# Performance work log

Measured on AMD Instinct MI355X. Metric: run time of the kernel, lower is better.

Reference implementation:

```python
import jax, jax.numpy as jnp
import numpy as np
from jax import lax

D_MODEL = 192; PATCH = 16; CH = 3
D_INNER = 384; D_STATE = 16; D_CONV = 4; DT_RANK = 12  # mamba_ssm defaults: expand=2, dt_rank=ceil(d_model/16)


def setup_inputs() -> dict:
    key = jax.random.key(0)
    ks = jax.random.split(key, 12)
    f32 = jnp.float32
    def rn(k, shape, s=0.02):
        return jax.random.normal(k, shape, f32) * s
    return {
        "x": jax.random.uniform(ks[0], (8, 3, 512, 512), f32),
        "patch_w": rn(ks[1], (D_MODEL, CH, PATCH, PATCH)),
        "patch_b": jnp.zeros((D_MODEL,), f32),
        "in_proj_w": rn(ks[2], (2 * D_INNER, D_MODEL)),
        "conv1d_w": rn(ks[3], (D_INNER, 1, D_CONV)),
        "conv1d_b": jnp.zeros((D_INNER,), f32),
        "x_proj_w": rn(ks[4], (DT_RANK + 2 * D_STATE, D_INNER)),
        "dt_proj_w": rn(ks[5], (D_INNER, DT_RANK)),
        "dt_proj_b": rn(ks[6], (D_INNER,), 0.1),
        "A_log": jnp.log(jnp.broadcast_to(jnp.arange(1, D_STATE + 1, dtype=f32), (D_INNER, D_STATE))),
        "D": jnp.ones((D_INNER,), f32),
        "out_proj_w": rn(ks[7], (D_MODEL, D_INNER)),
        "deconv_w": rn(ks[8], (D_MODEL, 64, PATCH, PATCH)),
        "deconv_b": jnp.zeros((64,), f32),
        "dec_conv_w": rn(ks[9], (CH, 64, 3, 3)),
        "dec_conv_b": jnp.zeros((CH,), f32),
    }


def _mamba(seq, in_proj_w, conv1d_w, conv1d_b, x_proj_w, dt_proj_w, dt_proj_b, A_log, D, out_proj_w):
    # seq: (B, L, d_model)
    B, L, _ = seq.shape
    xz = seq @ in_proj_w.T                              # (B, L, 2*d_inner)
    u, z = jnp.split(xz, 2, axis=-1)
    # depthwise causal conv1d (torch pads d_conv-1 both sides then truncates to L == left-pad only)
    uc = lax.conv_general_dilated(u.transpose(0, 2, 1), conv1d_w, (1,), [(D_CONV - 1, 0)],
                                  dimension_numbers=('NCH', 'OIH', 'NCH'),
                                  feature_group_count=D_INNER)       # (B, d_inner, L)
    u = jax.nn.silu((uc + conv1d_b[:, None]).transpose(0, 2, 1))     # (B, L, d_inner)
    dbc = u @ x_proj_w.T                                              # (B, L, dt_rank + 2*d_state)
    dt, Bm, Cm = jnp.split(dbc, [DT_RANK, DT_RANK + D_STATE], axis=-1)
    delta = jax.nn.softplus(dt @ dt_proj_w.T + dt_proj_b)            # (B, L, d_inner)
    A = -jnp.exp(A_log)                                               # (d_inner, d_state)
    dA = jnp.exp(delta[..., None] * A)                                # (B, L, d_inner, d_state)
    dBu = delta[..., None] * Bm[:, :, None, :] * u[..., None]         # (B, L, d_inner, d_state)
    def step(h, inp):
        a, b = inp
        h = a * h + b
        return h, h
    h0 = jnp.zeros((B, D_INNER, D_STATE), seq.dtype)
    _, hs = lax.scan(step, h0, (dA.transpose(1, 0, 2, 3), dBu.transpose(1, 0, 2, 3)))
    y = jnp.einsum('lbdn,bln->bld', hs, Cm) + u * D                   # (B, L, d_inner)
    y = y * jax.nn.silu(z)
    return y @ out_proj_w.T                                           # (B, L, d_model)


def reference(x, patch_w, patch_b, in_proj_w, conv1d_w, conv1d_b, x_proj_w,
              dt_proj_w, dt_proj_b, A_log, D, out_proj_w,
              deconv_w, deconv_b, dec_conv_w, dec_conv_b):
    B = x.shape[0]
    e = lax.conv_general_dilated(x, patch_w, (PATCH, PATCH), 'VALID',
                                 dimension_numbers=('NCHW', 'OIHW', 'NCHW')) + patch_b[:, None, None]
    h, w = e.shape[2], e.shape[3]
    seq = e.reshape(B, D_MODEL, h * w).transpose(0, 2, 1)             # (B, L, d_model)
    seq = _mamba(seq, in_proj_w, conv1d_w, conv1d_b, x_proj_w, dt_proj_w, dt_proj_b, A_log, D, out_proj_w)
    g = seq.transpose(0, 2, 1).reshape(B, D_MODEL, h, w)
    # ConvTranspose2d with stride == kernel_size is a non-overlapping patch expansion
    d = jnp.einsum('bchw,cdpq->bdhpwq', g, deconv_w).reshape(B, 64, h * PATCH, w * PATCH)
    d = jax.nn.relu(d + deconv_b[:, None, None])
    out = lax.conv_general_dilated(d, dec_conv_w, (1, 1), [(1, 1), (1, 1)],
                                   dimension_numbers=('NCHW', 'OIHW', 'NCHW')) + dec_conv_b[:, None, None]
    return jax.nn.sigmoid(out)
```

## Files before the change

kernel.cpp:

```cpp
#include <hip/hip_runtime.h>
#include <math.h>


typedef short bf16x8 __attribute__((ext_vector_type(8)));
typedef float f32x4 __attribute__((ext_vector_type(4)));

__device__ inline unsigned short f2bf(float f) {
    unsigned int u = __float_as_uint(f);
    unsigned int r = (u + 0x7fff + ((u >> 16) & 1)) >> 16;
    return (unsigned short)r;
}

__global__ __launch_bounds__(256) void gemm_mfma_flex(
    const unsigned short* __restrict__ A, const unsigned short* __restrict__ W,
    void* __restrict__ Cout, const float* __restrict__ bias,
    int M, int N, int K, int out_bf16)
{
    __shared__ unsigned short As[128][48];
    __shared__ unsigned short Bs[128][48];
    const int tid = threadIdx.x;
    const int wave = tid >> 6, lane = tid & 63;
    const int wm = (wave & 1) * 64, wn = (wave >> 1) * 64;
    const int m0 = blockIdx.y * 128, n0 = blockIdx.x * 128;
    const int quad = lane >> 4, lr = lane & 15;
    const uint4 z4 = {0, 0, 0, 0};

    f32x4 acc[4][4];
    #pragma unroll
    for (int i = 0; i < 4; ++i)
        #pragma unroll
        for (int j = 0; j < 4; ++j)
            acc[i][j] = (f32x4){0.f, 0.f, 0.f, 0.f};

    const int r = tid >> 2, kq = tid & 3;
    for (int k0 = 0; k0 < K; k0 += 32) {
        #pragma unroll
        for (int half = 0; half < 2; ++half) {
            int rr = r + half * 64;
            *(uint4*)(&As[rr][kq * 8]) =
                *(const uint4*)(A + (size_t)(m0 + rr) * K + k0 + kq * 8);
            uint4 bv = z4;
            if (n0 + rr < N)
                bv = *(const uint4*)(W + (size_t)(n0 + rr) * K + k0 + kq * 8);
            *(uint4*)(&Bs[rr][kq * 8]) = bv;
        }
        __syncthreads();
        bf16x8 af[4], bfr[4];
        #pragma unroll
        for (int i = 0; i < 4; ++i) af[i] = *(const bf16x8*)(&As[wm + i * 16 + lr][quad * 8]);
        #pragma unroll
        for (int j = 0; j < 4; ++j) bfr[j] = *(const bf16x8*)(&Bs[wn + j * 16 + lr][quad * 8]);
        #pragma unroll
        for (int i = 0; i < 4; ++i)
            #pragma unroll
            for (int j = 0; j < 4; ++j)
                acc[i][j] = __builtin_amdgcn_mfma_f32_16x16x32_bf16(af[i], bfr[j], acc[i][j], 0, 0, 0);
        __syncthreads();
    }

    #pragma unroll
    for (int i = 0; i < 4; ++i) {
        int gm = m0 + wm + i * 16 + quad * 4;
        #pragma unroll
        for (int j = 0; j < 4; ++j) {
            int gn = n0 + wn + j * 16 + lr;
            if (gn >= N) continue;
            float bv = bias ? bias[gn] : 0.f;
            #pragma unroll
            for (int rr = 0; rr < 4; ++rr) {
                float v = acc[i][j][rr] + bv;
                if (out_bf16) ((unsigned short*)Cout)[(size_t)(gm + rr) * N + gn] = f2bf(v);
                else          ((float*)Cout)[(size_t)(gm + rr) * N + gn] = v;
            }
        }
    }
}

__global__ __launch_bounds__(256) void gemm_mfma_relu_bf16(
    const unsigned short* __restrict__ A0, const unsigned short* __restrict__ W,
    unsigned short* __restrict__ C0, const float* __restrict__ bias, int pair)
{
    __shared__ unsigned short smem[12288];
    unsigned short* As = smem;
    unsigned short* Bs = smem + 6144;
    const int N = 16384, K = 192;
    const int tid = threadIdx.x;
    const int wave = tid >> 6, lane = tid & 63;
    const int wm = (wave & 1) * 64, wn = (wave >> 1) * 64;
    const int m0 = blockIdx.y * 128, n0 = blockIdx.x * 128;
    const int z = blockIdx.z;
    const unsigned short* A = A0 + (size_t)(pair * 2 + z) * 1024 * 192;
    unsigned short* C = C0 + (size_t)z * 16777216;
    const int quad = lane >> 4, lr = lane & 15;

    f32x4 acc[4][4];
    #pragma unroll
    for (int i = 0; i < 4; ++i)
        #pragma unroll
        for (int j = 0; j < 4; ++j)
            acc[i][j] = (f32x4){0.f, 0.f, 0.f, 0.f};

    const int r = tid >> 2, kq = tid & 3;
    for (int k0 = 0; k0 < K; k0 += 32) {
        #pragma unroll
        for (int half = 0; half < 2; ++half) {
            int rr = r + half * 64;
            *(uint4*)(&As[rr * 48 + kq * 8]) =
                *(const uint4*)(A + (size_t)(m0 + rr) * K + k0 + kq * 8);
            *(uint4*)(&Bs[rr * 48 + kq * 8]) =
                *(const uint4*)(W + (size_t)(n0 + rr) * K + k0 + kq * 8);
        }
        __syncthreads();
        bf16x8 af[4], bfr[4];
        #pragma unroll
        for (int i = 0; i < 4; ++i) af[i] = *(const bf16x8*)(&As[(wm + i * 16 + lr) * 48 + quad * 8]);
        #pragma unroll
        for (int j = 0; j < 4; ++j) bfr[j] = *(const bf16x8*)(&Bs[(wn + j * 16 + lr) * 48 + quad * 8]);
        #pragma unroll
        for (int i = 0; i < 4; ++i)
            #pragma unroll
            for (int j = 0; j < 4; ++j)
                acc[i][j] = __builtin_amdgcn_mfma_f32_16x16x32_bf16(af[i], bfr[j], acc[i][j], 0, 0, 0);
        __syncthreads();
    }

    unsigned short* Ct = smem;
    #pragma unroll
    for (int h = 0; h < 2; ++h) {
        if ((wave & 1) == h) {
            #pragma unroll
            for (int i = 0; i < 4; ++i) {
                int lrow = i * 16 + quad * 4;
                #pragma unroll
                for (int j = 0; j < 4; ++j) {
                    int lcol = wn + j * 16 + lr;
                    float bv = bias[(n0 + lcol) & 63];
                    #pragma unroll
                    for (int rr = 0; rr < 4; ++rr) {
                        float v = fmaxf(acc[i][j][rr] + bv, 0.f);
                        Ct[(lrow + rr) * 136 + lcol] = f2bf(v);
                    }
                }
            }
        }
        __syncthreads();
        #pragma unroll
        for (int p = 0; p < 4; ++p) {
            int idx = p * 256 + tid;
            int row = idx >> 4, cg = idx & 15;
            *(uint4*)(C + (size_t)(m0 + h * 64 + row) * N + n0 + cg * 8) =
                *(const uint4*)(&Ct[row * 136 + cg * 8]);
        }
        __syncthreads();
    }
}

__global__ __launch_bounds__(256) void im2col_bf16(const float* __restrict__ x,
                                                   unsigned short* __restrict__ P)
{
    int idx = blockIdx.x * 256 + threadIdx.x;
    int col = idx % 768;
    int row = idx / 768;
    int b = row >> 10;
    int l = row & 1023;
    int h = l >> 5, w = l & 31;
    int c = col >> 8;
    int p = (col >> 4) & 15, q = col & 15;
    P[idx] = f2bf(x[((size_t)(b * 3 + c) * 512 + (h * 16 + p)) * 512 + (w * 16 + q)]);
}

__global__ __launch_bounds__(256) void f2b_all(
    const float* __restrict__ a, unsigned short* __restrict__ da,
    const float* __restrict__ b, unsigned short* __restrict__ db,
    const float* __restrict__ c, unsigned short* __restrict__ dc,
    const float* __restrict__ d, unsigned short* __restrict__ dd)
{
    int i = blockIdx.x * 256 + threadIdx.x;
    if (i < 147456) da[i] = f2bf(a[i]);
    else if (i < 294912) db[i - 147456] = f2bf(b[i - 147456]);
    else if (i < 311808) dc[i - 294912] = f2bf(c[i - 294912]);
    else if (i < 385536) dd[i - 311808] = f2bf(d[i - 311808]);
}

__global__ __launch_bounds__(256) void conv1d_silu(const float* __restrict__ xz,
                                                   const float* __restrict__ cw,
                                                   const float* __restrict__ cb,
                                                   float* __restrict__ u32,
                                                   unsigned short* __restrict__ u16)
{
    int idx = blockIdx.x * 256 + threadIdx.x;
    int d = idx % 384;
    int row = idx / 384;
    int l = row & 1023;
    float acc = cb[d];
    #pragma unroll
    for (int j = 0; j < 4; ++j) {
        int ll = l - 3 + j;
        if (ll >= 0) acc += xz[(size_t)(row - 3 + j) * 768 + d] * cw[d * 4 + j];
    }
    float s = acc / (1.f + __expf(-acc));
    u32[idx] = s;
    u16[idx] = f2bf(s);
}

__global__ __launch_bounds__(256) void dtproj_softplus(const float* __restrict__ dbc,
                                                       const float* __restrict__ dtw,
                                                       const float* __restrict__ dtb,
                                                       float* __restrict__ delta)
{
    int idx = blockIdx.x * 256 + threadIdx.x;
    int n = idx % 384, m = idx / 384;
    const float* row = dbc + (size_t)m * 44;
    const float* wr  = dtw + n * 12;
    float acc = dtb[n];
    #pragma unroll
    for (int j = 0; j < 12; ++j) acc = fmaf(row[j], wr[j], acc);
    delta[idx] = (acc > 20.f) ? acc : log1pf(__expf(acc));
}

__global__ __launch_bounds__(256) void ssm_pass1(const float* __restrict__ delta,
                                                 const float* __restrict__ dbc,
                                                 const float* __restrict__ u,
                                                 const float* __restrict__ A_log,
                                                 float* __restrict__ Pc,
                                                 float* __restrict__ Hc)
{
    const int tid = threadIdx.x;
    const int n4 = tid & 3, dloc = tid >> 2;
    const int c = blockIdx.x, dg = blockIdx.y, b = blockIdx.z;
    const int d = dg * 64 + dloc;
    const int blk = (b * 6 + dg) * 32 + c;
    f32x4 A4 = *(const f32x4*)(A_log + d * 16 + n4 * 4);
    float Aa[4];
    #pragma unroll
    for (int j = 0; j < 4; ++j) Aa[j] = -__expf(A4[j]);
    const float* dp = delta + (size_t)(b * 1024) * 384 + d;
    const float* up = u     + (size_t)(b * 1024) * 384 + d;
    const float* bp = dbc   + (size_t)(b * 1024) * 44;
    float P[4] = {1.f, 1.f, 1.f, 1.f}, H[4] = {0.f, 0.f, 0.f, 0.f};
    const int l0 = c * 32;
    for (int l = l0; l < l0 + 32; ++l) {
        float dlv = dp[(size_t)l * 384];
        float ulv = up[(size_t)l * 384];
        f32x4 B4 = *(const f32x4*)(bp + (size_t)l * 44 + 12 + n4 * 4);
        float du = dlv * ulv;
        #pragma unroll
        for (int j = 0; j < 4; ++j) {
            float a = __expf(dlv * Aa[j]);
            P[j] *= a;
            H[j] = fmaf(a, H[j], du * B4[j]);
        }
    }
    size_t o = ((size_t)blk * 256 + tid) * 4;
    *(f32x4*)(Pc + o) = (f32x4){P[0], P[1], P[2], P[3]};
    *(f32x4*)(Hc + o) = (f32x4){H[0], H[1], H[2], H[3]};
}

__global__ __launch_bounds__(256) void ssm_pass2(const float* __restrict__ Pc,
                                                 const float* __restrict__ Hc,
                                                 float* __restrict__ h0c)
{
    int t = blockIdx.x * 256 + threadIdx.x;
    int grp = t >> 10, dn = t & 1023;
    float h = 0.f;
    #pragma unroll
    for (int c = 0; c < 32; ++c) {
        size_t idx = ((size_t)(grp * 32 + c)) * 1024 + dn;
        h0c[idx] = h;
        h = fmaf(Pc[idx], h, Hc[idx]);
    }
}

__global__ __launch_bounds__(256) void ssm_pass3(const float* __restrict__ delta,
                                                 const float* __restrict__ dbc,
                                                 const float* __restrict__ u,
                                                 const float* __restrict__ xz,
                                                 const float* __restrict__ A_log,
                                                 const float* __restrict__ Dp,
                                                 const float* __restrict__ h0c,
                                                 unsigned short* __restrict__ y16)
{
    const int tid = threadIdx.x;
    const int n4 = tid & 3, dloc = tid >> 2;
    const int c = blockIdx.x, dg = blockIdx.y, b = blockIdx.z;
    const int d = dg * 64 + dloc;
    const int blk = (b * 6 + dg) * 32 + c;
    f32x4 A4 = *(const f32x4*)(A_log + d * 16 + n4 * 4);
    float Aa[4];
    #pragma unroll
    for (int j = 0; j < 4; ++j) Aa[j] = -__expf(A4[j]);
    float Dv = Dp[d];
    const float* dp = delta + (size_t)(b * 1024) * 384 + d;
    const float* up = u     + (size_t)(b * 1024) * 384 + d;
    const float* bp = dbc   + (size_t)(b * 1024) * 44;
    const float* zp = xz    + (size_t)(b * 1024) * 768 + 384 + d;
    unsigned short* yp = y16 + (size_t)(b * 1024) * 384 + d;
    f32x4 h4 = *(const f32x4*)(h0c + ((size_t)blk * 256 + tid) * 4);
    float H[4] = {h4[0], h4[1], h4[2], h4[3]};
    const int l0 = c * 32;
    for (int l = l0; l < l0 + 32; ++l) {
        float dlv = dp[(size_t)l * 384];
        float ulv = up[(size_t)l * 384];
        f32x4 B4 = *(const f32x4*)(bp + (size_t)l * 44 + 12 + n4 * 4);
        f32x4 C4 = *(const f32x4*)(bp + (size_t)l * 44 + 28 + n4 * 4);
        float du = dlv * ulv;
        float part = 0.f;
        #pragma unroll
        for (int j = 0; j < 4; ++j) {
            float a = __expf(dlv * Aa[j]);
            H[j] = fmaf(a, H[j], du * B4[j]);
            part = fmaf(H[j], C4[j], part);
        }
        part += __shfl_xor(part, 1, 4);
        part += __shfl_xor(part, 2, 4);
        if (n4 == 0) {
            float z = zp[(size_t)l * 768];
            float sz = z / (1.f + __expf(-z));
            yp[(size_t)l * 384] = f2bf((part + ulv * Dv) * sz);
        }
    }
}

__global__ __launch_bounds__(256) void transpose_w_bf16(const float* __restrict__ src,
                                                        unsigned short* __restrict__ dst)
{
    int idx = blockIdx.x * 256 + threadIdx.x;
    int c = idx % 192;
    int np = idx / 192;
    int k = np & 63;
    int pq = np >> 6;
    dst[idx] = f2bf(src[(size_t)c * 16384 + k * 256 + pq]);
}

__global__ void prep_wconv(const float* __restrict__ w, unsigned short* __restrict__ wc)
{
    int i = blockIdx.x * 256 + threadIdx.x;
    if (i >= 9216) return;
    int ch = i & 63;
    int m = (i >> 6) & 15;
    int tap = i >> 10;
    int dy = tap / 3, dx = tap % 3;
    float v = (m < 3) ? w[((m * 64 + ch) * 3 + dy) * 3 + dx] : 0.f;
    wc[i] = f2bf(v);
}

__global__ __launch_bounds__(256) void decconv_mfma(
    const unsigned short* __restrict__ Db, const unsigned short* __restrict__ wconv,
    const float* __restrict__ dcb, float* __restrict__ out, int pair)
{
    __shared__ unsigned short ds[18 * 18 * 72];
    const int t = threadIdx.x;
    const int pidx = blockIdx.x;
    const int bb = blockIdx.y;
    const int b = pair * 2 + bb;
    const unsigned short* Dbb = Db + (size_t)bb * 16777216;
    const int ph = pidx >> 5, pw = pidx & 31;
    const uint4 z4 = {0, 0, 0, 0};

    const unsigned short* base = Dbb + ((size_t)pidx << 14);
    #pragma unroll
    for (int s = 0; s < 8; ++s) {
        int f = s * 256 + t;
        int k8 = f & 7, pq = f >> 3;
        *(uint4*)&ds[(((pq >> 4) + 1) * 18 + (pq & 15) + 1) * 72 + k8 * 8] =
            *(const uint4*)(base + pq * 64 + k8 * 8);
    }
    {
        int k8 = t & 7, e = (t >> 3) & 15;
        if (t < 128) {
            uint4 v = z4;
            if (ph > 0) v = *(const uint4*)(Dbb + ((size_t)(pidx - 32) << 14) + (240 + e) * 64 + k8 * 8);
            *(uint4*)&ds[(0 * 18 + e + 1) * 72 + k8 * 8] = v;
        } else {
            uint4 v = z4;
            if (ph < 31) v = *(const uint4*)(Dbb + ((size_t)(pidx + 32) << 14) + e * 64 + k8 * 8);
            *(uint4*)&ds[(17 * 18 + e + 1) * 72 + k8 * 8] = v;
        }
        if (t < 128) {
            uint4 v = z4;
            if (pw > 0) v = *(const uint4*)(Dbb + ((size_t)(pidx - 1) << 14) + (e * 16 + 15) * 64 + k8 * 8);
            *(uint4*)&ds[((e + 1) * 18 + 0) * 72 + k8 * 8] = v;
        } else {
            uint4 v = z4;
            if (pw < 31) v = *(const uint4*)(Dbb + ((size_t)(pidx + 1) << 14) + (e * 16) * 64 + k8 * 8);
            *(uint4*)&ds[((e + 1) * 18 + 17) * 72 + k8 * 8] = v;
        }
        if (t < 32) {
            int c = t >> 3;
            int dh = (c >> 1) * 2 - 1, dw = (c & 1) * 2 - 1;
            int nh = ph + dh, nw = pw + dw;
            int sp = dh < 0 ? 15 : 0, sq = dw < 0 ? 15 : 0;
            uint4 v = z4;
            if (nh >= 0 && nh < 32 && nw >= 0 && nw < 32)
                v = *(const uint4*)(Dbb + ((size_t)(nh * 32 + nw) << 14) + (sp * 16 + sq) * 64 + k8 * 8);
            int dy = dh < 0 ? 0 : 17, dx = dw < 0 ? 0 : 17;
            *(uint4*)&ds[(dy * 18 + dx) * 72 + k8 * 8] = v;
        }
    }
    __syncthreads();

    const int wave = t >> 6, lane = t & 63;
    const int quad = lane >> 4, lr = lane & 15;
    f32x4 acc[4];
    #pragma unroll
    for (int i = 0; i < 4; ++i) acc[i] = (f32x4){0.f, 0.f, 0.f, 0.f};

    #pragma unroll
    for (int tap = 0; tap < 9; ++tap) {
        const int dy = tap / 3, dx = tap % 3;
        bf16x8 a0 = *(const bf16x8*)(wconv + (tap * 16 + lr) * 64 + quad * 8);
        bf16x8 a1 = *(const bf16x8*)(wconv + (tap * 16 + lr) * 64 + 32 + quad * 8);
        #pragma unroll
        for (int i = 0; i < 4; ++i) {
            int p = wave * 4 + i;
            const unsigned short* cell = &ds[((p + dy) * 18 + lr + dx) * 72];
            bf16x8 b0 = *(const bf16x8*)(cell + quad * 8);
            bf16x8 b1 = *(const bf16x8*)(cell + 32 + quad * 8);
            acc[i] = __builtin_amdgcn_mfma_f32_16x16x32_bf16(a0, b0, acc[i], 0, 0, 0);
            acc[i] = __builtin_amdgcn_mfma_f32_16x16x32_bf16(a1, b1, acc[i], 0, 0, 0);
        }
    }

    if (quad == 0) {
        float b0 = dcb[0], b1 = dcb[1], b2 = dcb[2];
        #pragma unroll
        for (int i = 0; i < 4; ++i) {
            int Y = ph * 16 + wave * 4 + i, X = pw * 16 + lr;
            size_t o = (size_t)(b * 3) * 262144 + (size_t)Y * 512 + X;
            out[o]          = 1.f / (1.f + __expf(-(acc[i][0] + b0)));
            out[o + 262144] = 1.f / (1.f + __expf(-(acc[i][1] + b1)));
            out[o + 524288] = 1.f / (1.f + __expf(-(acc[i][2] + b2)));
        }
    }
}

#define WS_P16      0
#define WS_DELTA    0
#define WS_SEQ16    3145728
#define WS_DBC      3145728
#define WS_XZ       3932160
#define WS_U32      10223616
#define WS_U16      13369344
#define WS_Y16      13369344
#define WS_PC       14155776
#define WS_HC       15728640
#define WS_H0C      17301504
#define WS_DB       0
#define WS_SEQOB    16777216
#define WS_W2       17563648
#define WS_WP16     19136512
#define WS_WI16     19210240
#define WS_WX16     19283968
#define WS_WO16     19292416
#define WS_WCONV    19329280

extern "C" void kernel_launch(void* const* d_in, const int* in_sizes, int n_in,
                              void* d_out, int out_size, void* d_ws, size_t ws_size,
                              hipStream_t stream)
{
    const float* x         = (const float*)d_in[0];
    const float* patch_w   = (const float*)d_in[1];
    const float* patch_b   = (const float*)d_in[2];
    const float* in_proj_w = (const float*)d_in[3];
    const float* conv1d_w  = (const float*)d_in[4];
    const float* conv1d_b  = (const float*)d_in[5];
    const float* x_proj_w  = (const float*)d_in[6];
    const float* dt_proj_w = (const float*)d_in[7];
    const float* dt_proj_b = (const float*)d_in[8];
    const float* A_log     = (const float*)d_in[9];
    const float* Dp        = (const float*)d_in[10];
    const float* out_proj_w= (const float*)d_in[11];
    const float* deconv_w  = (const float*)d_in[12];
    const float* deconv_b  = (const float*)d_in[13];
    const float* dec_conv_w= (const float*)d_in[14];
    const float* dec_conv_b= (const float*)d_in[15];
    float* out = (float*)d_out;
    float* ws  = (float*)d_ws;

    unsigned short* P16   = (unsigned short*)(ws + WS_P16);
    float*          delta = ws + WS_DELTA;
    unsigned short* seq16 = (unsigned short*)(ws + WS_SEQ16);
    float*          dbc   = ws + WS_DBC;
    float*          xz    = ws + WS_XZ;
    float*          u32   = ws + WS_U32;
    unsigned short* u16   = (unsigned short*)(ws + WS_U16);
    unsigned short* y16   = (unsigned short*)(ws + WS_Y16);
    float*          Pc    = ws + WS_PC;
    float*          Hc    = ws + WS_HC;
    float*          h0c   = ws + WS_H0C;
    unsigned short* Db16  = (unsigned short*)(ws + WS_DB);
    unsigned short* seqo_b= (unsigned short*)(ws + WS_SEQOB);
    unsigned short* W2b   = (unsigned short*)(ws + WS_W2);
    unsigned short* wp16  = (unsigned short*)(ws + WS_WP16);
    unsigned short* wi16  = (unsigned short*)(ws + WS_WI16);
    unsigned short* wx16  = (unsigned short*)(ws + WS_WX16);
    unsigned short* wo16  = (unsigned short*)(ws + WS_WO16);
    unsigned short* wconv = (unsigned short*)(ws + WS_WCONV);

    im2col_bf16<<<24576, 256, 0, stream>>>(x, P16);
    f2b_all<<<1506, 256, 0, stream>>>(patch_w, wp16, in_proj_w, wi16,
                                      x_proj_w, wx16, out_proj_w, wo16);
    gemm_mfma_flex<<<dim3(2, 64), 256, 0, stream>>>(P16, wp16, seq16, patch_b,
                                                    8192, 192, 768, 1);
    gemm_mfma_flex<<<dim3(6, 64), 256, 0, stream>>>(seq16, wi16, xz, nullptr,
                                                    8192, 768, 192, 0);
    conv1d_silu<<<12288, 256, 0, stream>>>(xz, conv1d_w, conv1d_b, u32, u16);
    gemm_mfma_flex<<<dim3(1, 64), 256, 0, stream>>>(u16, wx16, dbc, nullptr,
                                                    8192, 44, 384, 0);
    dtproj_softplus<<<12288, 256, 0, stream>>>(dbc, dt_proj_w, dt_proj_b, delta);
    ssm_pass1<<<dim3(32, 6, 8), 256, 0, stream>>>(delta, dbc, u32, A_log, Pc, Hc);
    ssm_pass2<<<192, 256, 0, stream>>>(Pc, Hc, h0c);
    ssm_pass3<<<dim3(32, 6, 8), 256, 0, stream>>>(delta, dbc, u32, xz, A_log, Dp, h0c, y16);
    gemm_mfma_flex<<<dim3(2, 64), 256, 0, stream>>>(y16, wo16, seqo_b, nullptr,
                                                    8192, 192, 384, 1);
    transpose_w_bf16<<<12288, 256, 0, stream>>>(deconv_w, W2b);
    prep_wconv<<<36, 256, 0, stream>>>(dec_conv_w, wconv);
    for (int pair = 0; pair < 4; ++pair) {
        gemm_mfma_relu_bf16<<<dim3(128, 8, 2), 256, 0, stream>>>(
            seqo_b, W2b, Db16, deconv_b, pair);
        decconv_mfma<<<dim3(1024, 2), 256, 0, stream>>>(Db16, wconv, dec_conv_b, out, pair);
    }
}
```

Measured before the change: 551.4 us.

## Fuse prep kernels, fold dt_proj into x_proj GEMM, store xz in bf16, batch decoder groups

All conversion and transpose prep kernels (im2col, weight casts, deconv weight transpose, wconv packing) are merged into one launch. dt_proj is folded algebraically into the x_proj weight, so a single GEMM produces delta with softplus plus a compact B/C buffer. The xz intermediate is stored as bf16 instead of fp32, which halves its traffic. The decoder loop processes 4 batches per group instead of 2 when the workspace is large enough, cutting launches. This adds risk from bf16 rounding of z/u and from the precomputed dt·x_proj product in bf16.

```diff
diff --git a/kernel.cpp b/kernel.cpp
--- a/kernel.cpp
+++ b/kernel.cpp
@@ -9,6 +9,9 @@
     unsigned int u = __float_as_uint(f);
     unsigned int r = (u + 0x7fff + ((u >> 16) & 1)) >> 16;
     return (unsigned short)r;
+}
+__device__ inline float bf2f(unsigned short s) {
+    return __uint_as_float(((unsigned int)s) << 16);
 }
 
 __global__ __launch_bounds__(256) void gemm_mfma_flex(
@@ -76,9 +79,79 @@
     }
 }
 
+__global__ __launch_bounds__(256) void gemm_xd(
+    const unsigned short* __restrict__ A, const unsigned short* __restrict__ W,
+    float* __restrict__ delta, float* __restrict__ bc,
+    const float* __restrict__ dtb)
+{
+    __shared__ unsigned short As[128][48];
+    __shared__ unsigned short Bs[128][48];
+    const int N = 416, K = 384;
+    const int tid = threadIdx.x;
+    const int wave = tid >> 6, lane = tid & 63;
+    const int wm = (wave & 1) * 64, wn = (wave >> 1) * 64;
+    const int m0 = blockIdx.y * 128, n0 = blockIdx.x * 128;
+    const int quad = lane >> 4, lr = lane & 15;
+    const uint4 z4 = {0, 0, 0, 0};
+
+    f32x4 acc[4][4];
+    #pragma unroll
+    for (int i = 0; i < 4; ++i)
+        #pragma unroll
+        for (int j = 0; j < 4; ++j)
+            acc[i][j] = (f32x4){0.f, 0.f, 0.f, 0.f};
+
+    const int r = tid >> 2, kq = tid & 3;
+    for (int k0 = 0; k0 < K; k0 += 32) {
+        #pragma unroll
+        for (int half = 0; half < 2; ++half) {
+            int rr = r + half * 64;
+            *(uint4*)(&As[rr][kq * 8]) =
+                *(const uint4*)(A + (size_t)(m0 + rr) * K + k0 + kq * 8);
+            uint4 bv = z4;
+            if (n0 + rr < N)
+                bv = *(const uint4*)(W + (size_t)(n0 + rr) * K + k0 + kq * 8);
+            *(uint4*)(&Bs[rr][kq * 8]) = bv;
+        }
+        __syncthreads();
+        bf16x8 af[4], bfr[4];
+        #pragma unroll
+        for (int i = 0; i < 4; ++i) af[i] = *(const bf16x8*)(&As[wm + i * 16 + lr][quad * 8]);
+        #pragma unroll
+        for (int j = 0; j < 4; ++j) bfr[j] = *(const bf16x8*)(&Bs[wn + j * 16 + lr][quad * 8]);
+        #pragma unroll
+        for (int i = 0; i < 4; ++i)
+            #pragma unroll
+            for (int j = 0; j < 4; ++j)
+                acc[i][j] = __builtin_amdgcn_mfma_f32_16x16x32_bf16(af[i], bfr[j], acc[i][j], 0, 0, 0);
+        __syncthreads();
+    }
+
+    #pragma unroll
+    for (int i = 0; i < 4; ++i) {
+        int gm = m0 + wm + i * 16 + quad * 4;
+        #pragma unroll
+        for (int j = 0; j < 4; ++j) {
+            int gn = n0 + wn + j * 16 + lr;
+            if (gn >= N) continue;
+            #pragma unroll
+            for (int rr = 0; rr < 4; ++rr) {
+                float v = acc[i][j][rr];
+                if (gn < 384) {
+                    v += dtb[gn];
+                    v = (v > 20.f) ? v : log1pf(__expf(v));
+                    delta[(size_t)(gm + rr) * 384 + gn] = v;
+                } else {
+                    bc[(size_t)(gm + rr) * 32 + gn - 384] = v;
+                }
+            }
+        }
+    }
+}
+
 __global__ __launch_bounds__(256) void gemm_mfma_relu_bf16(
     const unsigned short* __restrict__ A0, const unsigned short* __restrict__ W,
-    unsigned short* __restrict__ C0, const float* __restrict__ bias, int pair)
+    unsigned short* __restrict__ C0, const float* __restrict__ bias, int base_b)
 {
     __shared__ unsigned short smem[12288];
     unsigned short* As = smem;
@@ -89,7 +162,7 @@
     const int wm = (wave & 1) * 64, wn = (wave >> 1) * 64;
     const int m0 = blockIdx.y * 128, n0 = blockIdx.x * 128;
     const int z = blockIdx.z;
-    const unsigned short* A = A0 + (size_t)(pair * 2 + z) * 1024 * 192;
+    const unsigned short* A = A0 + (size_t)(base_b + z) * 1024 * 192;
     unsigned short* C = C0 + (size_t)z * 16777216;
     const int quad = lane >> 4, lr = lane & 15;
 
@@ -155,34 +228,63 @@
     }
 }
 
-__global__ __launch_bounds__(256) void im2col_bf16(const float* __restrict__ x,
-                                                   unsigned short* __restrict__ P)
-{
-    int idx = blockIdx.x * 256 + threadIdx.x;
-    int col = idx % 768;
-    int row = idx / 768;
-    int b = row >> 10;
-    int l = row & 1023;
-    int h = l >> 5, w = l & 31;
-    int c = col >> 8;
-    int p = (col >> 4) & 15, q = col & 15;
-    P[idx] = f2bf(x[((size_t)(b * 3 + c) * 512 + (h * 16 + p)) * 512 + (w * 16 + q)]);
-}
-
-__global__ __launch_bounds__(256) void f2b_all(
-    const float* __restrict__ a, unsigned short* __restrict__ da,
-    const float* __restrict__ b, unsigned short* __restrict__ db,
-    const float* __restrict__ c, unsigned short* __restrict__ dc,
-    const float* __restrict__ d, unsigned short* __restrict__ dd)
+__global__ __launch_bounds__(256) void prep_all(
+    const float* __restrict__ x, unsigned short* __restrict__ P,
+    const float* __restrict__ patch_w, unsigned short* __restrict__ wp,
+    const float* __restrict__ in_proj_w, unsigned short* __restrict__ wi,
+    const float* __restrict__ out_proj_w, unsigned short* __restrict__ wo,
+    const float* __restrict__ deconv_w, unsigned short* __restrict__ W2,
+    const float* __restrict__ dec_conv_w, unsigned short* __restrict__ wconv,
+    const float* __restrict__ dtw, const float* __restrict__ xpw,
+    unsigned short* __restrict__ wxd)
 {
     int i = blockIdx.x * 256 + threadIdx.x;
-    if (i < 147456) da[i] = f2bf(a[i]);
-    else if (i < 294912) db[i - 147456] = f2bf(b[i - 147456]);
-    else if (i < 311808) dc[i - 294912] = f2bf(c[i - 294912]);
-    else if (i < 385536) dd[i - 311808] = f2bf(d[i - 311808]);
-}
-
-__global__ __launch_bounds__(256) void conv1d_silu(const float* __restrict__ xz,
+    if (i < 6291456) {
+        int col = i % 768, row = i / 768;
+        int b = row >> 10, l = row & 1023;
+        int h = l >> 5, w = l & 31;
+        int c = col >> 8, p = (col >> 4) & 15, q = col & 15;
+        P[i] = f2bf(x[((size_t)(b * 3 + c) * 512 + (h * 16 + p)) * 512 + (w * 16 + q)]);
+        return;
+    }
+    i -= 6291456;
+    if (i < 147456) { wp[i] = f2bf(patch_w[i]); return; }
+    i -= 147456;
+    if (i < 147456) { wi[i] = f2bf(in_proj_w[i]); return; }
+    i -= 147456;
+    if (i < 73728) { wo[i] = f2bf(out_proj_w[i]); return; }
+    i -= 73728;
+    if (i < 3145728) {
+        int c = i % 192, np = i / 192;
+        int k = np & 63, pq = np >> 6;
+        W2[i] = f2bf(deconv_w[(size_t)c * 16384 + k * 256 + pq]);
+        return;
+    }
+    i -= 3145728;
+    if (i < 9216) {
+        int ch = i & 63, m = (i >> 6) & 15, tap = i >> 10;
+        int dy = tap / 3, dx = tap % 3;
+        float v = (m < 3) ? dec_conv_w[((m * 64 + ch) * 3 + dy) * 3 + dx] : 0.f;
+        wconv[i] = f2bf(v);
+        return;
+    }
+    i -= 9216;
+    {
+        int col = i % 384, row = i / 384;
+        float v;
+        if (row < 384) {
+            v = 0.f;
+            #pragma unroll
+            for (int j = 0; j < 12; ++j)
+                v = fmaf(dtw[row * 12 + j], xpw[j * 384 + col], v);
+        } else {
+            v = xpw[(row - 384 + 12) * 384 + col];
+        }
+        wxd[i] = f2bf(v);
+    }
+}
+
+__global__ __launch_bounds__(256) void conv1d_silu(const unsigned short* __restrict__ xz,
                                                    const float* __restrict__ cw,
                                                    const float* __restrict__ cb,
                                                    float* __restrict__ u32,
@@ -196,30 +298,15 @@
     #pragma unroll
     for (int j = 0; j < 4; ++j) {
         int ll = l - 3 + j;
-        if (ll >= 0) acc += xz[(size_t)(row - 3 + j) * 768 + d] * cw[d * 4 + j];
+        if (ll >= 0) acc += bf2f(xz[(size_t)(row - 3 + j) * 768 + d]) * cw[d * 4 + j];
     }
     float s = acc / (1.f + __expf(-acc));
     u32[idx] = s;
     u16[idx] = f2bf(s);
 }
 
-__global__ __launch_bounds__(256) void dtproj_softplus(const float* __restrict__ dbc,
-                                                       const float* __restrict__ dtw,
-                                                       const float* __restrict__ dtb,
-                                                       float* __restrict__ delta)
-{
-    int idx = blockIdx.x * 256 + threadIdx.x;
-    int n = idx % 384, m = idx / 384;
-    const float* row = dbc + (size_t)m * 44;
-    const float* wr  = dtw + n * 12;
-    float acc = dtb[n];
-    #pragma unroll
-    for (int j = 0; j < 12; ++j) acc = fmaf(row[j], wr[j], acc);
-    delta[idx] = (acc > 20.f) ? acc : log1pf(__expf(acc));
-}
-
 __global__ __launch_bounds__(256) void ssm_pass1(const float* __restrict__ delta,
-                                                 const float* __restrict__ dbc,
+                                                 const float* __restrict__ bc,
                                                  const float* __restrict__ u,
                                                  const float* __restrict__ A_log,
                                                  float* __restrict__ Pc,
@@ -236,13 +323,13 @@
     for (int j = 0; j < 4; ++j) Aa[j] = -__expf(A4[j]);
     const float* dp = delta + (size_t)(b * 1024) * 384 + d;
     const float* up = u     + (size_t)(b * 1024) * 384 + d;
-    const float* bp = dbc   + (size_t)(b * 1024) * 44;
+    const float* bp = bc    + (size_t)(b * 1024) * 32;
     float P[4] = {1.f, 1.f, 1.f, 1.f}, H[4] = {0.f, 0.f, 0.f, 0.f};
     const int l0 = c * 32;
     for (int l = l0; l < l0 + 32; ++l) {
         float dlv = dp[(size_t)l * 384];
         float ulv = up[(size_t)l * 384];
-        f32x4 B4 = *(const f32x4*)(bp + (size_t)l * 44 + 12 + n4 * 4);
+        f32x4 B4 = *(const f32x4*)(bp + (size_t)l * 32 + n4 * 4);
         float du = dlv * ulv;
         #pragma unroll
         for (int j = 0; j < 4; ++j) {
@@ -272,9 +359,9 @@
 }
 
 __global__ __launch_bounds__(256) void ssm_pass3(const float* __restrict__ delta,
-                                                 const float* __restrict__ dbc,
+                                                 const float* __restrict__ bc,
                                                  const float* __restrict__ u,
-                                                 const float* __restrict__ xz,
+                                                 const unsigned short* __restrict__ xz,
                                                  const float* __restrict__ A_log,
                                                  const float* __restrict__ Dp,
                                                  const float* __restrict__ h0c,
@@ -292,8 +379,8 @@
     float Dv = Dp[d];
     const float* dp = delta + (size_t)(b * 1024) * 384 + d;
     const float* up = u     + (size_t)(b * 1024) * 384 + d;
-    const float* bp = dbc   + (size_t)(b * 1024) * 44;
-    const float* zp = xz    + (size_t)(b * 1024) * 768 + 384 + d;
+    const float* bp = bc    + (size_t)(b * 1024) * 32;
+    const unsigned short* zp = xz + (size_t)(b * 1024) * 768 + 384 + d;
     unsigned short* yp = y16 + (size_t)(b * 1024) * 384 + d;
     f32x4 h4 = *(const f32x4*)(h0c + ((size_t)blk * 256 + tid) * 4);
     float H[4] = {h4[0], h4[1], h4[2], h4[3]};
@@ -301,8 +388,8 @@
     for (int l = l0; l < l0 + 32; ++l) {
         float dlv = dp[(size_t)l * 384];
         float ulv = up[(size_t)l * 384];
-        f32x4 B4 = *(const f32x4*)(bp + (size_t)l * 44 + 12 + n4 * 4);
-        f32x4 C4 = *(const f32x4*)(bp + (size_t)l * 44 + 28 + n4 * 4);
+        f32x4 B4 = *(const f32x4*)(bp + (size_t)l * 32 + n4 * 4);
+        f32x4 C4 = *(const f32x4*)(bp + (size_t)l * 32 + 16 + n4 * 4);
         float du = dlv * ulv;
         float part = 0.f;
         #pragma unroll
@@ -314,45 +401,22 @@
         part += __shfl_xor(part, 1, 4);
         part += __shfl_xor(part, 2, 4);
         if (n4 == 0) {
-            float z = zp[(size_t)l * 768];
+            float z = bf2f(zp[(size_t)l * 768]);
             float sz = z / (1.f + __expf(-z));
             yp[(size_t)l * 384] = f2bf((part + ulv * Dv) * sz);
         }
     }
 }
 
-__global__ __launch_bounds__(256) void transpose_w_bf16(const float* __restrict__ src,
-                                                        unsigned short* __restrict__ dst)
-{
-    int idx = blockIdx.x * 256 + threadIdx.x;
-    int c = idx % 192;
-    int np = idx / 192;
-    int k = np & 63;
-    int pq = np >> 6;
-    dst[idx] = f2bf(src[(size_t)c * 16384 + k * 256 + pq]);
-}
-
-__global__ void prep_wconv(const float* __restrict__ w, unsigned short* __restrict__ wc)
-{
-    int i = blockIdx.x * 256 + threadIdx.x;
-    if (i >= 9216) return;
-    int ch = i & 63;
-    int m = (i >> 6) & 15;
-    int tap = i >> 10;
-    int dy = tap / 3, dx = tap % 3;
-    float v = (m < 3) ? w[((m * 64 + ch) * 3 + dy) * 3 + dx] : 0.f;
-    wc[i] = f2bf(v);
-}
-
 __global__ __launch_bounds__(256) void decconv_mfma(
     const unsigned short* __restrict__ Db, const unsigned short* __restrict__ wconv,
-    const float* __restrict__ dcb, float* __restrict__ out, int pair)
+    const float* __restrict__ dcb, float* __restrict__ out, int base_b)
 {
     __shared__ unsigned short ds[18 * 18 * 72];
     const int t = threadIdx.x;
     const int pidx = blockIdx.x;
     const int bb = blockIdx.y;
-    const int b = pair * 2 + bb;
+    const int b = base_b + bb;
     const unsigned short* Dbb = Db + (size_t)bb * 16777216;
     const int ph = pidx >> 5, pw = pidx & 31;
     const uint4 z4 = {0, 0, 0, 0};
@@ -437,22 +501,14 @@
 #define WS_P16      0
 #define WS_DELTA    0
 #define WS_SEQ16    3145728
-#define WS_DBC      3145728
-#define WS_XZ       3932160
-#define WS_U32      10223616
-#define WS_U16      13369344
-#define WS_Y16      13369344
-#define WS_PC       14155776
-#define WS_HC       15728640
-#define WS_H0C      17301504
-#define WS_DB       0
-#define WS_SEQOB    16777216
-#define WS_W2       17563648
-#define WS_WP16     19136512
-#define WS_WI16     19210240
-#define WS_WX16     19283968
-#define WS_WO16     19292416
-#define WS_WCONV    19329280
+#define WS_XZ16     3538944
+#define WS_U32      6684672
+#define WS_U16      9830400
+#define WS_Y16      9830400
+#define WS_BC       10223616
+#define WS_PC       10485760
+#define WS_HC       12058624
+#define WS_H0C      13631488
 
 extern "C" void kernel_launch(void* const* d_in, const int* in_sizes, int n_in,
                               void* d_out, int out_size, void* d_ws, size_t ws_size,
@@ -477,47 +533,46 @@
     float* out = (float*)d_out;
     float* ws  = (float*)d_ws;
 
+    const int G = (ws_size >= (size_t)143157248) ? 4 : 2;
+    const size_t wbase = (G == 4) ? 33554432 : 16777216;
+
     unsigned short* P16   = (unsigned short*)(ws + WS_P16);
     float*          delta = ws + WS_DELTA;
     unsigned short* seq16 = (unsigned short*)(ws + WS_SEQ16);
-    float*          dbc   = ws + WS_DBC;
-    float*          xz    = ws + WS_XZ;
+    unsigned short* xz16  = (unsigned short*)(ws + WS_XZ16);
     float*          u32   = ws + WS_U32;
     unsigned short* u16   = (unsigned short*)(ws + WS_U16);
     unsigned short* y16   = (unsigned short*)(ws + WS_Y16);
+    float*          bc    = ws + WS_BC;
     float*          Pc    = ws + WS_PC;
     float*          Hc    = ws + WS_HC;
     float*          h0c   = ws + WS_H0C;
-    unsigned short* Db16  = (unsigned short*)(ws + WS_DB);
-    unsigned short* seqo_b= (unsigned short*)(ws + WS_SEQOB);
-    unsigned short* W2b   = (unsigned short*)(ws + WS_W2);
-    unsigned short* wp16  = (unsigned short*)(ws + WS_WP16);
-    unsigned short* wi16  = (unsigned short*)(ws + WS_WI16);
-    unsigned short* wx16  = (unsigned short*)(ws + WS_WX16);
-    unsigned short* wo16  = (unsigned short*)(ws + WS_WO16);
-    unsigned short* wconv = (unsigned short*)(ws + WS_WCONV);
-
-    im2col_bf16<<<24576, 256, 0, stream>>>(x, P16);
-    f2b_all<<<1506, 256, 0, stream>>>(patch_w, wp16, in_proj_w, wi16,
-                                      x_proj_w, wx16, out_proj_w, wo16);
+    unsigned short* Db16  = (unsigned short*)(ws);
+    unsigned short* seqo_b= (unsigned short*)(ws + wbase);
+    unsigned short* W2b   = (unsigned short*)(ws + wbase + 393216);
+    unsigned short* wconv = (unsigned short*)(ws + wbase + 1966080);
+    unsigned short* wp16  = (unsigned short*)(ws + wbase + 1970688);
+    unsigned short* wi16  = (unsigned short*)(ws + wbase + 2044416);
+    unsigned short* wo16  = (unsigned short*)(ws + wbase + 2118144);
+    unsigned short* wxd   = (unsigned short*)(ws + wbase + 2155008);
+
+    prep_all<<<38964, 256, 0, stream>>>(x, P16, patch_w, wp16, in_proj_w, wi16,
+                                        out_proj_w, wo16, deconv_w, W2b,
+                                        dec_conv_w, wconv, dt_proj_w, x_proj_w, wxd);
     gemm_mfma_flex<<<dim3(2, 64), 256, 0, stream>>>(P16, wp16, seq16, patch_b,
                                                     8192, 192, 768, 1);
-    gemm_mfma_flex<<<dim3(6, 64), 256, 0, stream>>>(seq16, wi16, xz, nullptr,
-                                                    8192, 768, 192, 0);
-    conv1d_silu<<<12288, 256, 0, stream>>>(xz, conv1d_w, conv1d_b, u32, u16);
-    gemm_mfma_flex<<<dim3(1, 64), 256, 0, stream>>>(u16, wx16, dbc, nullptr,
-                                                    8192, 44, 384, 0);
-    dtproj_softplus<<<12288, 256, 0, stream>>>(dbc, dt_proj_w, dt_proj_b, delta);
-    ssm_pass1<<<dim3(32, 6, 8), 256, 0, stream>>>(delta, dbc, u32, A_log, Pc, Hc);
+    gemm_mfma_flex<<<dim3(6, 64), 256, 0, stream>>>(seq16, wi16, xz16, nullptr,
+                                                    8192, 768, 192, 1);
+    conv1d_silu<<<12288, 256, 0, stream>>>(xz16, conv1d_w, conv1d_b, u32, u16);
+    gemm_xd<<<dim3(4, 64), 256, 0, stream>>>(u16, wxd, delta, bc, dt_proj_b);
+    ssm_pass1<<<dim3(32, 6, 8), 256, 0, stream>>>(delta, bc, u32, A_log, Pc, Hc);
     ssm_pass2<<<192, 256, 0, stream>>>(Pc, Hc, h0c);
-    ssm_pass3<<<dim3(32, 6, 8), 256, 0, stream>>>(delta, dbc, u32, xz, A_log, Dp, h0c, y16);
+    ssm_pass3<<<dim3(32, 6, 8), 256, 0, stream>>>(delta, bc, u32, xz16, A_log, Dp, h0c, y16);
     gemm_mfma_flex<<<dim3(2, 64), 256, 0, stream>>>(y16, wo16, seqo_b, nullptr,
                                                     8192, 192, 384, 1);
-    transpose_w_bf16<<<12288, 256, 0, stream>>>(deconv_w, W2b);
-    prep_wconv<<<36, 256, 0, stream>>>(dec_conv_w, wconv);
-    for (int pair = 0; pair < 4; ++pair) {
-        gemm_mfma_relu_bf16<<<dim3(128, 8, 2), 256, 0, stream>>>(
-            seqo_b, W2b, Db16, deconv_b, pair);
-        decconv_mfma<<<dim3(1024, 2), 256, 0, stream>>>(Db16, wconv, dec_conv_b, out, pair);
-    }
-}
+    for (int g = 0; g < 8 / G; ++g) {
+        gemm_mfma_relu_bf16<<<dim3(128, 8, G), 256, 0, stream>>>(
+            seqo_b, W2b, Db16, deconv_b, g * G);
+        decconv_mfma<<<dim3(1024, G), 256, 0, stream>>>(Db16, wconv, dec_conv_b, out, g * G);
+    }
+}
```

Result: faster. 535.1 us (-3.0%).
